# Kernel optimization log

Measured on AMD Instinct MI355X. Metric: run time of the kernel, lower is better.

Reference implementation:

```python
import jax, jax.numpy as jnp
import numpy as np

CORE_DIM = 128
MEMORY_SLOTS = 64
B, S = 4, 4096


def setup_inputs() -> dict:
    key = jax.random.key(0)
    k1, k2, k3, k4, k5 = jax.random.split(key, 5)
    x = jax.random.normal(k1, (B, S, CORE_DIM), dtype=jnp.float32)
    memory_keys = jax.random.normal(k2, (MEMORY_SLOTS, CORE_DIM), dtype=jnp.float32)
    memory_ops = jax.random.normal(k3, (MEMORY_SLOTS, CORE_DIM, CORE_DIM), dtype=jnp.float32)
    # nn.Linear(core_dim, core_dim): weight [out, in], bias [out]
    bound = 1.0 / np.sqrt(CORE_DIM)
    Wq = jax.random.uniform(k4, (CORE_DIM, CORE_DIM), minval=-bound, maxval=bound, dtype=jnp.float32)
    bq = jax.random.uniform(k5, (CORE_DIM,), minval=-bound, maxval=bound, dtype=jnp.float32)
    return {"input_tensor": x, "memory_keys": memory_keys, "memory_ops": memory_ops, "Wq": Wq, "bq": bq}


def reference(input_tensor, memory_keys, memory_ops, Wq, bq):
    dim = input_tensor.shape[-1]
    # query projection: x @ Wq^T + bq
    queries = jnp.einsum('bsd,ed->bse', input_tensor, Wq) + bq
    # soft attention over memory slots
    attn_logits = jnp.einsum('bsd,md->bsm', queries, memory_keys)
    attn_weights = jax.nn.softmax(attn_logits / jnp.sqrt(jnp.float32(dim)), axis=-1)
    # fused: (sum_m attn[bsm] * ops[m]) @ x[bs]  == sum_m attn[bsm] * (ops[m] @ x[bs])
    processed = jnp.einsum('bsm,mde,bse->bsd', attn_weights, memory_ops, input_tensor)
    return processed
```

## Files before the change

### kernel.cpp

```cpp
#include <hip/hip_runtime.h>

typedef __bf16 bf16x8 __attribute__((ext_vector_type(8)));
typedef float f32x4 __attribute__((ext_vector_type(4)));
typedef unsigned int uint4v __attribute__((ext_vector_type(4)));
typedef unsigned short ushort_t;
typedef unsigned int uint_t;

#define RS 0.08838834764831845f

__device__ __forceinline__ ushort_t f2bf(float f) {
    uint_t u = __float_as_uint(f);
    u += 0x7FFFu + ((u >> 16) & 1u);
    return (ushort_t)(u >> 16);
}
__device__ __forceinline__ uint_t pack2(float a, float b) {
    return (uint_t)f2bf(a) | ((uint_t)f2bf(b) << 16);
}
union U4B8 { uint4v u; bf16x8 b; };
__device__ __forceinline__ bf16x8 as_bf(uint4v u) { U4B8 x; x.u = u; return x.b; }

__device__ __forceinline__ void pf16(const void* g, void* l) {
    __builtin_amdgcn_global_load_lds(
        (const __attribute__((address_space(1))) void*)g,
        (__attribute__((address_space(3))) void*)l, 16, 0, 0);
}

__device__ __forceinline__ int xfrag(int f, int lane) {
    return f * 1072 + ((lane >> 4) * 272) + ((lane & 15) * 16);
}

__global__ __launch_bounds__(256) void prep_kernel(
    const float* __restrict__ ops, const float* __restrict__ keys,
    const float* __restrict__ Wq, const float* __restrict__ bq,
    uint4v* __restrict__ ops_sw, ushort_t* __restrict__ kp_sw,
    float* __restrict__ cb)
{
    const int tid = threadIdx.x;
    const int b = blockIdx.x;
    if (b >= 64) {
        int g = (b - 64) * 256 + tid;
        int L = g & 63, dt = (g >> 6) & 7, ks = (g >> 9) & 3, m = g >> 11;
        int d = dt * 16 + (L & 15);
        int e0 = ks * 32 + ((L >> 4) << 3);
        const float4* s = (const float4*)(ops + (((size_t)(m * 128 + d)) << 7) + e0);
        float4 v0 = s[0], v1 = s[1];
        uint4v o = { pack2(v0.x, v0.y), pack2(v0.z, v0.w),
                     pack2(v1.x, v1.y), pack2(v1.z, v1.w) };
        ops_sw[g] = o;
    } else {
        __shared__ float red[256];
        const int m = b;
        const int d = tid & 127, eh = tid >> 7;
        const float* kr = keys + m * 128 + eh * 64;
        const float* wc = Wq + (size_t)(eh * 64) * 128 + d;
        float acc = 0.f;
        #pragma unroll 8
        for (int e = 0; e < 64; ++e)
            acc = fmaf(kr[e], wc[(size_t)e * 128], acc);
        red[tid] = acc;
        __syncthreads();
        if (tid < 128) {
            float v = red[tid] + red[tid + 128];
            int ki = d >> 5, qq = (d >> 3) & 3, j = d & 7;
            kp_sw[((((ki * 4 + (m >> 4)) * 64) + (qq * 16 + (m & 15))) << 3) | j] = f2bf(v);
        } else if (tid >= 192) {
            int lane = tid - 192;
            float p = keys[m * 128 + lane] * bq[lane]
                    + keys[m * 128 + 64 + lane] * bq[64 + lane];
            #pragma unroll
            for (int off = 1; off < 64; off <<= 1) p += __shfl_xor(p, off);
            if (lane == 0) cb[m] = p;
        }
    }
}

__global__ __launch_bounds__(256, 2) void main_kernel(
    const float* __restrict__ x, const float* __restrict__ cb,
    const ushort_t* __restrict__ kp_sw, const uint4v* __restrict__ ops_sw,
    float* __restrict__ out)
{
    __shared__ __align__(16) unsigned char xs[17152];
    __shared__ __align__(16) unsigned char bb[4][2][4096];
    __shared__ float attn_f[64 * 68];

    const int tid = threadIdx.x;
    const int lane = tid & 63;
    const int w = tid >> 6;
    const int q = lane >> 4;
    const int l15 = lane & 15;
    const int tb = blockIdx.x >> 1;
    const int dh = blockIdx.x & 1;
    const int t0 = tb * 64;
    const int dtw = dh * 4 + w;

    {
        const float4* x4 = (const float4*)(x + (size_t)t0 * 128);
        #pragma unroll
        for (int it = 0; it < 4; ++it) {
            int i = it * 256 + tid;
            int t = i >> 4, kc = i & 15;
            float4 a = x4[t * 32 + kc * 2];
            float4 b2 = x4[t * 32 + kc * 2 + 1];
            uint4v o = { pack2(a.x, a.y), pack2(a.z, a.w),
                         pack2(b2.x, b2.y), pack2(b2.z, b2.w) };
            *(uint4v*)(xs + ((t >> 4) * 4 + (kc >> 2)) * 1072
                          + (kc & 3) * 272 + (t & 15) * 16) = o;
        }
    }
    __syncthreads();

    const char* obase = (const char*)ops_sw + ((size_t)(dtw * 64 + lane) << 4);
    unsigned char* bw = &bb[w][0][0];
    #pragma unroll
    for (int ki = 0; ki < 4; ++ki)
        pf16(obase + ki * 8192, bw + ki * 1024);

    {
        f32x4 L0 = {0,0,0,0}, L1 = {0,0,0,0}, L2 = {0,0,0,0}, L3 = {0,0,0,0};
        const uint4v* kpf = (const uint4v*)kp_sw;
        #pragma unroll
        for (int ki = 0; ki < 4; ++ki) {
            bf16x8 a = *(const bf16x8*)(xs + xfrag(w * 4 + ki, lane));
            L0 = __builtin_amdgcn_mfma_f32_16x16x32_bf16(a, as_bf(kpf[(ki*4+0)*64 + lane]), L0, 0,0,0);
            L1 = __builtin_amdgcn_mfma_f32_16x16x32_bf16(a, as_bf(kpf[(ki*4+1)*64 + lane]), L1, 0,0,0);
            L2 = __builtin_amdgcn_mfma_f32_16x16x32_bf16(a, as_bf(kpf[(ki*4+2)*64 + lane]), L2, 0,0,0);
            L3 = __builtin_amdgcn_mfma_f32_16x16x32_bf16(a, as_bf(kpf[(ki*4+3)*64 + lane]), L3, 0,0,0);
        }
        float c0 = cb[l15], c1 = cb[16 + l15], c2 = cb[32 + l15], c3 = cb[48 + l15];
        #pragma unroll
        for (int r = 0; r < 4; ++r) {
            float v0 = (L0[r] + c0) * RS;
            float v1 = (L1[r] + c1) * RS;
            float v2 = (L2[r] + c2) * RS;
            float v3 = (L3[r] + c3) * RS;
            float mx = fmaxf(fmaxf(v0, v1), fmaxf(v2, v3));
            #pragma unroll
            for (int off = 1; off < 16; off <<= 1) mx = fmaxf(mx, __shfl_xor(mx, off));
            float e0 = __expf(v0 - mx), e1 = __expf(v1 - mx),
                  e2 = __expf(v2 - mx), e3 = __expf(v3 - mx);
            float sm = e0 + e1 + e2 + e3;
            #pragma unroll
            for (int off = 1; off < 16; off <<= 1) sm += __shfl_xor(sm, off);
            float inv = 1.0f / sm;
            int t = w * 16 + q * 4 + r;
            attn_f[(     l15) * 68 + t] = e0 * inv;
            attn_f[(16 + l15) * 68 + t] = e1 * inv;
            attn_f[(32 + l15) * 68 + t] = e2 * inv;
            attn_f[(48 + l15) * 68 + t] = e3 * inv;
        }
    }

    bf16x8 A[4][4];
    #pragma unroll
    for (int tf = 0; tf < 4; ++tf)
        #pragma unroll
        for (int ki = 0; ki < 4; ++ki)
            A[tf][ki] = *(const bf16x8*)(xs + xfrag(tf * 4 + ki, lane));

    __syncthreads();

    f32x4 C[4] = {};
    for (int ml = 0; ml < 64; ++ml) {
        const int cur = ml & 1;
        if (ml < 63) {
            const char* src = obase + ((size_t)(ml + 1) << 15);
            unsigned char* dst = bw + (cur ^ 1) * 4096;
            #pragma unroll
            for (int ki = 0; ki < 4; ++ki)
                pf16(src + ki * 8192, dst + ki * 1024);
            __builtin_amdgcn_s_waitcnt(0x0F74);
        } else {
            __builtin_amdgcn_s_waitcnt(0x0F70);
        }
        __builtin_amdgcn_sched_barrier(0);

        bf16x8 b0 = *(const bf16x8*)(bw + cur * 4096 +    0 + lane * 16);
        bf16x8 b1 = *(const bf16x8*)(bw + cur * 4096 + 1024 + lane * 16);
        bf16x8 b2 = *(const bf16x8*)(bw + cur * 4096 + 2048 + lane * 16);
        bf16x8 b3 = *(const bf16x8*)(bw + cur * 4096 + 3072 + lane * 16);

        f32x4 S[4] = {};
        #pragma unroll
        for (int tf = 0; tf < 4; ++tf) {
            S[tf] = __builtin_amdgcn_mfma_f32_16x16x32_bf16(A[tf][0], b0, S[tf], 0,0,0);
            S[tf] = __builtin_amdgcn_mfma_f32_16x16x32_bf16(A[tf][1], b1, S[tf], 0,0,0);
            S[tf] = __builtin_amdgcn_mfma_f32_16x16x32_bf16(A[tf][2], b2, S[tf], 0,0,0);
            S[tf] = __builtin_amdgcn_mfma_f32_16x16x32_bf16(A[tf][3], b3, S[tf], 0,0,0);
        }
        #pragma unroll
        for (int tf = 0; tf < 4; ++tf) {
            f32x4 af = *(const f32x4*)&attn_f[ml * 68 + tf * 16 + q * 4];
            #pragma unroll
            for (int r = 0; r < 4; ++r)
                C[tf][r] = fmaf(af[r], S[tf][r], C[tf][r]);
        }
    }

    float* op = out + (size_t)t0 * 128 + dh * 64 + w * 16 + l15;
    #pragma unroll
    for (int tf = 0; tf < 4; ++tf)
        #pragma unroll
        for (int r = 0; r < 4; ++r)
            op[(size_t)(tf * 16 + q * 4 + r) * 128] = C[tf][r];
}

extern "C" void kernel_launch(void* const* d_in, const int* in_sizes, int n_in,
                              void* d_out, int out_size, void* d_ws, size_t ws_size,
                              hipStream_t stream)
{
    const float* x    = (const float*)d_in[0];
    const float* keys = (const float*)d_in[1];
    const float* ops  = (const float*)d_in[2];
    const float* Wq   = (const float*)d_in[3];
    const float* bq   = (const float*)d_in[4];
    float* out = (float*)d_out;

    char* ws = (char*)d_ws;
    uint4v*   ops_sw = (uint4v*)ws;
    ushort_t* kp_sw  = (ushort_t*)(ws + 2097152);
    float*    cb     = (float*)(ws + 2097152 + 16384);

    prep_kernel<<<576, 256, 0, stream>>>(ops, keys, Wq, bq, ops_sw, kp_sw, cb);
    main_kernel<<<512, 256, 0, stream>>>(x, cb, kp_sw, ops_sw, out);
}
```

Measured before the change: 119.0 us.

## Replace LDS double-buffered ops prefetch with register double-buffered global loads

Result: no change. 120.0 us (+0.8%).

```diff
diff --git a/kernel.cpp b/kernel.cpp
--- a/kernel.cpp
+++ b/kernel.cpp
@@ -18,12 +18,6 @@
 }
 union U4B8 { uint4v u; bf16x8 b; };
 __device__ __forceinline__ bf16x8 as_bf(uint4v u) { U4B8 x; x.u = u; return x.b; }
-
-__device__ __forceinline__ void pf16(const void* g, void* l) {
-    __builtin_amdgcn_global_load_lds(
-        (const __attribute__((address_space(1))) void*)g,
-        (__attribute__((address_space(3))) void*)l, 16, 0, 0);
-}
 
 __device__ __forceinline__ int xfrag(int f, int lane) {
     return f * 1072 + ((lane >> 4) * 272) + ((lane & 15) * 16);
@@ -80,7 +74,6 @@
     float* __restrict__ out)
 {
     __shared__ __align__(16) unsigned char xs[17152];
-    __shared__ __align__(16) unsigned char bb[4][2][4096];
     __shared__ float attn_f[64 * 68];
 
     const int tid = threadIdx.x;
@@ -109,12 +102,6 @@
     }
     __syncthreads();
 
-    const char* obase = (const char*)ops_sw + ((size_t)(dtw * 64 + lane) << 4);
-    unsigned char* bw = &bb[w][0][0];
-    #pragma unroll
-    for (int ki = 0; ki < 4; ++ki)
-        pf16(obase + ki * 8192, bw + ki * 1024);
-
     {
         f32x4 L0 = {0,0,0,0}, L1 = {0,0,0,0}, L2 = {0,0,0,0}, L3 = {0,0,0,0};
         const uint4v* kpf = (const uint4v*)kp_sw;
@@ -159,40 +146,53 @@
 
     __syncthreads();
 
+    const uint4v* ob = ops_sw + (size_t)dtw * 64 + lane;
     f32x4 C[4] = {};
-    for (int ml = 0; ml < 64; ++ml) {
-        const int cur = ml & 1;
-        if (ml < 63) {
-            const char* src = obase + ((size_t)(ml + 1) << 15);
-            unsigned char* dst = bw + (cur ^ 1) * 4096;
-            #pragma unroll
-            for (int ki = 0; ki < 4; ++ki)
-                pf16(src + ki * 8192, dst + ki * 1024);
-            __builtin_amdgcn_s_waitcnt(0x0F74);
-        } else {
-            __builtin_amdgcn_s_waitcnt(0x0F70);
-        }
-        __builtin_amdgcn_sched_barrier(0);
-
-        bf16x8 b0 = *(const bf16x8*)(bw + cur * 4096 +    0 + lane * 16);
-        bf16x8 b1 = *(const bf16x8*)(bw + cur * 4096 + 1024 + lane * 16);
-        bf16x8 b2 = *(const bf16x8*)(bw + cur * 4096 + 2048 + lane * 16);
-        bf16x8 b3 = *(const bf16x8*)(bw + cur * 4096 + 3072 + lane * 16);
-
-        f32x4 S[4] = {};
-        #pragma unroll
-        for (int tf = 0; tf < 4; ++tf) {
-            S[tf] = __builtin_amdgcn_mfma_f32_16x16x32_bf16(A[tf][0], b0, S[tf], 0,0,0);
-            S[tf] = __builtin_amdgcn_mfma_f32_16x16x32_bf16(A[tf][1], b1, S[tf], 0,0,0);
-            S[tf] = __builtin_amdgcn_mfma_f32_16x16x32_bf16(A[tf][2], b2, S[tf], 0,0,0);
-            S[tf] = __builtin_amdgcn_mfma_f32_16x16x32_bf16(A[tf][3], b3, S[tf], 0,0,0);
-        }
-        #pragma unroll
-        for (int tf = 0; tf < 4; ++tf) {
-            f32x4 af = *(const f32x4*)&attn_f[ml * 68 + tf * 16 + q * 4];
-            #pragma unroll
-            for (int r = 0; r < 4; ++r)
-                C[tf][r] = fmaf(af[r], S[tf][r], C[tf][r]);
+    uint4v B0[4], B1[4];
+    #pragma unroll
+    for (int ki = 0; ki < 4; ++ki) B0[ki] = ob[ki * 512];
+
+    for (int ml = 0; ml < 64; ml += 2) {
+        {
+            const uint4v* pn = ob + (size_t)(ml + 1) * 2048;
+            #pragma unroll
+            for (int ki = 0; ki < 4; ++ki) B1[ki] = pn[ki * 512];
+            f32x4 S[4] = {};
+            #pragma unroll
+            for (int ki = 0; ki < 4; ++ki) {
+                bf16x8 bfrag = as_bf(B0[ki]);
+                #pragma unroll
+                for (int tf = 0; tf < 4; ++tf)
+                    S[tf] = __builtin_amdgcn_mfma_f32_16x16x32_bf16(A[tf][ki], bfrag, S[tf], 0,0,0);
+            }
+            #pragma unroll
+            for (int tf = 0; tf < 4; ++tf) {
+                f32x4 af = *(const f32x4*)&attn_f[ml * 68 + tf * 16 + q * 4];
+                #pragma unroll
+                for (int r = 0; r < 4; ++r)
+                    C[tf][r] = fmaf(af[r], S[tf][r], C[tf][r]);
+            }
+        }
+        {
+            const int mn = (ml + 2 < 64) ? ml + 2 : 63;
+            const uint4v* pn = ob + (size_t)mn * 2048;
+            #pragma unroll
+            for (int ki = 0; ki < 4; ++ki) B0[ki] = pn[ki * 512];
+            f32x4 S[4] = {};
+            #pragma unroll
+            for (int ki = 0; ki < 4; ++ki) {
+                bf16x8 bfrag = as_bf(B1[ki]);
+                #pragma unroll
+                for (int tf = 0; tf < 4; ++tf)
+                    S[tf] = __builtin_amdgcn_mfma_f32_16x16x32_bf16(A[tf][ki], bfrag, S[tf], 0,0,0);
+            }
+            #pragma unroll
+            for (int tf = 0; tf < 4; ++tf) {
+                f32x4 af = *(const f32x4*)&attn_f[(ml + 1) * 68 + tf * 16 + q * 4];
+                #pragma unroll
+                for (int r = 0; r < 4; ++r)
+                    C[tf][r] = fmaf(af[r], S[tf][r], C[tf][r]);
+            }
         }
     }
 
```
